# Kernel tuning notes

Measured on AMD Instinct MI355X. Metric: run time of the kernel, lower is better.

Reference implementation:

```python
import jax, jax.numpy as jnp
import numpy as np

# Regular (dv=3, dc=6) LDPC Tanner graph, rate 1/2
N = 2097152   # variable nodes (code.n)
M = 1048576   # check nodes (H.shape[0])
DV = 3
DC = 6
T = 10        # max_iterations
BC = 4        # c2v bit-width -> 2^(bc-1) = 8 magnitude levels
K = 2 ** (BC - 1)
QUANT_PARAMS = [(2.0, 1.0), (4.0, 1.5), (6.0, 2.0)]


def _make_thresholds():
    """Per-iteration threshold table [T, K]; tau_j = C*(j/(K-1))**gamma."""
    def thr(C, g):
        return [C * (j / (K - 1)) ** g for j in range(K)]
    rows = []
    for t in range(T):
        if t < T // 3:
            C, g = QUANT_PARAMS[0]
        elif t < 2 * T // 3:
            C, g = QUANT_PARAMS[1]
        else:
            C, g = QUANT_PARAMS[-1]
        rows.append(thr(C, g))
    return jnp.asarray(rows, dtype=jnp.float32)


def setup_inputs() -> dict:
    key = jax.random.key(0)
    k_llr, k_beta, k_alpha = jax.random.split(key, 3)
    rng = np.random.default_rng(0)
    # each variable node has exactly DV edges; each check exactly DC edges
    var_idx = np.repeat(np.arange(N, dtype=np.int32), DV)
    chk_idx = rng.permutation(np.repeat(np.arange(M, dtype=np.int32), DC)).astype(np.int32)
    llr = jax.random.normal(k_llr, (N,), dtype=jnp.float32) * 2.0
    # weight init matches nn.Parameter(torch.randn(1)*0.1), one per (iter, degree)
    beta = jax.random.normal(k_beta, (T,), dtype=jnp.float32) * 0.1
    alpha = jax.random.normal(k_alpha, (T,), dtype=jnp.float32) * 0.1
    return {
        "llr": llr,
        "var_idx": jnp.asarray(var_idx),
        "chk_idx": jnp.asarray(chk_idx),
        "beta": beta,
        "alpha": alpha,
        "thresholds": _make_thresholds(),
        "m": M,
    }


def reference(llr, var_idx, chk_idx, beta, alpha, thresholds, m):
    n = llr.shape[0]
    E = var_idx.shape[0]
    eidx = jnp.arange(E, dtype=jnp.int32)
    INF = jnp.float32(jnp.inf)

    def step(v2c, xs):
        b, a, thr = xs  # scalar beta_t, alpha_t, thr [K]
        neg = v2c < 0
        sgn = jnp.where(neg, -1.0, 1.0).astype(v2c.dtype)
        mag = jnp.abs(v2c)
        # --- check node update: min-sum with exclusion (min1/min2) ---
        min1 = jax.ops.segment_min(mag, chk_idx, num_segments=m)
        # first edge attaining the min in each check (ties -> lowest edge id)
        cand = jnp.where(mag <= min1[chk_idx], eidx, E)
        first = jax.ops.segment_min(cand, chk_idx, num_segments=m)
        is_min = eidx == first[chk_idx]
        min2 = jax.ops.segment_min(jnp.where(is_min, INF, mag), chk_idx, num_segments=m)
        min2 = jnp.where(jnp.isinf(min2), min1, min2)  # degree-1 guard
        # sign product excluding self: total parity * own sign
        cnt = jax.ops.segment_sum(neg.astype(jnp.int32), chk_idx, num_segments=m)
        tot = (1 - 2 * (cnt & 1)).astype(v2c.dtype)
        sign_excl = tot[chk_idx] * sgn
        mval = jnp.where(is_min, min2[chk_idx], min1[chk_idx])
        raw = b * sign_excl * mval
        # --- RCQ quantize/dequantize of c2v: snap |raw| down to threshold ---
        q = jnp.clip(jnp.searchsorted(thr, jnp.abs(raw), side="right") - 1, 0, K - 1)
        c2v = jnp.where(raw < 0, -1.0, 1.0) * thr[q]
        # --- variable node update ---
        post = llr + jax.ops.segment_sum(c2v, var_idx, num_segments=n)
        v2c_new = a * (post[var_idx] - c2v)
        return v2c_new, post

    v2c0 = llr[var_idx]
    _, posts = jax.lax.scan(step, v2c0, (beta, alpha, thresholds))
    posterior = posts[-1]
    decoded = (posterior < 0).astype(jnp.int32)
    return decoded, posterior, jnp.int32(beta.shape[0])
```

## Files before the change

kernel.cpp:

```cpp
#include <hip/hip_runtime.h>
#include <stdint.h>

#define NV 2097152
#define MC 1048576
#define EE 6291456
#define TT 10

#define CHUNK 8192
#define NBLK 768
#define FBK 512
#define CPB 2048
#define CSEG 12288
#define FG 512
#define GSEG 12288
#define VBK 256
#define VSEG 24576

__global__ __launch_bounds__(512) void initcur_kernel(uint32_t* __restrict__ gcur) {
    int i = blockIdx.x * 512 + threadIdx.x;
    gcur[i] = (uint32_t)(i & 511) * 12288u;
}

__global__ __launch_bounds__(512) void bin1_kernel(const int* __restrict__ chk_idx,
                                                   uint32_t* __restrict__ gcurA,
                                                   uint32_t* __restrict__ im1_e,
                                                   uint16_t* __restrict__ im1_c) {
    __shared__ uint32_t cnt0[512];
    __shared__ uint32_t aux[512];
    __shared__ uint32_t sA[CHUNK];
    __shared__ uint16_t sB[CHUNK];
    const int tid = threadIdx.x;
    const int rep = tid >> 8;
    const int base = blockIdx.x * CHUNK;
    cnt0[tid] = 0; aux[tid] = 0;
    __syncthreads();
    int4 cc4[4];
#pragma unroll
    for (int k = 0; k < 4; ++k) cc4[k] = ((const int4*)chk_idx)[(base >> 2) + tid + 512 * k];
    uint32_t br[16];
#pragma unroll
    for (int k = 0; k < 4; ++k) {
        int cv[4] = {cc4[k].x, cc4[k].y, cc4[k].z, cc4[k].w};
#pragma unroll
        for (int ii = 0; ii < 4; ++ii) {
            uint32_t b = (uint32_t)cv[ii] >> 11;
            uint32_t r = atomicAdd(rep ? &aux[b] : &cnt0[b], 1u);
            br[k * 4 + ii] = (b << 13) | r;
        }
    }
    __syncthreads();
    const uint32_t s0 = cnt0[tid] + aux[tid];
    aux[tid] = s0;
    __syncthreads();
    for (int d = 1; d < 512; d <<= 1) {
        uint32_t a0 = (tid >= d) ? aux[tid - d] : 0u;
        __syncthreads();
        aux[tid] += a0;
        __syncthreads();
    }
    const uint32_t excl0 = aux[tid] - s0;
    aux[tid] = excl0;
    const uint32_t gb0 = atomicAdd(&gcurA[tid], s0);
    __syncthreads();
#pragma unroll
    for (int k = 0; k < 4; ++k) {
        int cv[4] = {cc4[k].x, cc4[k].y, cc4[k].z, cc4[k].w};
#pragma unroll
        for (int ii = 0; ii < 4; ++ii) {
            uint32_t v = br[k * 4 + ii];
            uint32_t b = v >> 13;
            uint32_t r = v & 8191u;
            uint32_t j = aux[b] + (rep ? cnt0[b] : 0u) + r;
            uint32_t e = (uint32_t)(base + (tid + 512 * k) * 4 + ii);
            sA[j] = (b << 23) | e;
            sB[j] = (uint16_t)((uint32_t)cv[ii] & 2047u);
        }
    }
    __syncthreads();
    aux[tid] = gb0 - excl0;
    __syncthreads();
#pragma unroll 8
    for (int k = 0; k < 16; ++k) {
        int j = tid + 512 * k;
        uint32_t v = sA[j];
        uint32_t b = v >> 23;
        uint32_t addr = aux[b] + (uint32_t)j;
        im1_e[addr] = v & 0x7FFFFFu;
        im1_c[addr] = sB[j];
    }
}

__global__ __launch_bounds__(1024) void place1_kernel(const uint32_t* __restrict__ im1_e,
                                                      const uint16_t* __restrict__ im1_c,
                                                      uint32_t* __restrict__ chk_edges,
                                                      uint8_t* __restrict__ b1rank,
                                                      uint32_t* __restrict__ runcntB) {
    __shared__ uint32_t win[CSEG];
    __shared__ uint32_t ccnt[CPB / 2];
    __shared__ uint32_t cntB[VBK];
    const int tid = threadIdx.x, blk = blockIdx.x;
    ccnt[tid] = 0;
    if (tid < VBK) cntB[tid] = 0;
    __syncthreads();
    const size_t cb = (size_t)blk * CSEG;
    for (int k = 0; k < 3; ++k) {
        int j0 = (tid + 1024 * k) * 4;
        const uint4 e4 = *(const uint4*)&im1_e[cb + j0];
        const ushort4 c4 = *(const ushort4*)&im1_c[cb + j0];
        uint32_t c, old, s;
        c = c4.x; old = atomicAdd(&ccnt[c >> 1], 1u << ((c & 1) * 16));
        s = (old >> ((c & 1) * 16)) & 0xFFFFu; win[c * 6 + s] = e4.x;
        c = c4.y; old = atomicAdd(&ccnt[c >> 1], 1u << ((c & 1) * 16));
        s = (old >> ((c & 1) * 16)) & 0xFFFFu; win[c * 6 + s] = e4.y;
        c = c4.z; old = atomicAdd(&ccnt[c >> 1], 1u << ((c & 1) * 16));
        s = (old >> ((c & 1) * 16)) & 0xFFFFu; win[c * 6 + s] = e4.z;
        c = c4.w; old = atomicAdd(&ccnt[c >> 1], 1u << ((c & 1) * 16));
        s = (old >> ((c & 1) * 16)) & 0xFFFFu; win[c * 6 + s] = e4.w;
    }
    __syncthreads();
    for (int j = tid; j < CSEG; j += 1024) chk_edges[cb + j] = win[j];
    for (int k = 0; k < CSEG / 1024; ++k) {
        int lp = tid + 1024 * k;
        uint32_t e = win[lp];
        uint32_t bB = (e / 3u) >> 13;
        uint32_t r = atomicAdd(&cntB[bB], 1u);
        b1rank[cb + lp] = (uint8_t)r;
    }
    __syncthreads();
    if (tid < VBK) runcntB[(size_t)tid * FBK + blk] = cntB[tid];
}

__global__ __launch_bounds__(512) void bin2_kernel(const uint32_t* __restrict__ chk_edges,
                                                   uint32_t* __restrict__ gcurB,
                                                   uint32_t* __restrict__ im2_pay,
                                                   uint16_t* __restrict__ im2_el) {
    __shared__ uint32_t cnt0[512];
    __shared__ uint32_t aux[512];
    __shared__ uint32_t sA[CHUNK];
    __shared__ uint16_t sB[CHUNK];
    const int tid = threadIdx.x;
    const int rep = tid >> 8;
    const int base = blockIdx.x * CHUNK;
    cnt0[tid] = 0; aux[tid] = 0;
    __syncthreads();
    uint4 ee4[4];
#pragma unroll
    for (int k = 0; k < 4; ++k) ee4[k] = ((const uint4*)chk_edges)[(base >> 2) + tid + 512 * k];
    uint32_t br[16];
#pragma unroll
    for (int k = 0; k < 4; ++k) {
        uint32_t ev[4] = {ee4[k].x, ee4[k].y, ee4[k].z, ee4[k].w};
#pragma unroll
        for (int ii = 0; ii < 4; ++ii) {
            uint32_t vb = ev[ii] / 12288u;
            uint32_t r = atomicAdd(rep ? &aux[vb] : &cnt0[vb], 1u);
            br[k * 4 + ii] = (vb << 13) | r;
        }
    }
    __syncthreads();
    const uint32_t s0 = cnt0[tid] + aux[tid];
    aux[tid] = s0;
    __syncthreads();
    for (int d = 1; d < 512; d <<= 1) {
        uint32_t a0 = (tid >= d) ? aux[tid - d] : 0u;
        __syncthreads();
        aux[tid] += a0;
        __syncthreads();
    }
    const uint32_t excl0 = aux[tid] - s0;
    aux[tid] = excl0;
    const uint32_t gb0 = atomicAdd(&gcurB[tid], s0);
    __syncthreads();
#pragma unroll
    for (int k = 0; k < 4; ++k) {
        uint32_t ev[4] = {ee4[k].x, ee4[k].y, ee4[k].z, ee4[k].w};
#pragma unroll
        for (int ii = 0; ii < 4; ++ii) {
            uint32_t v = br[k * 4 + ii];
            uint32_t vb = v >> 13;
            uint32_t r = v & 8191u;
            uint32_t j = aux[vb] + (rep ? cnt0[vb] : 0u) + r;
            uint32_t pl = (uint32_t)((tid + 512 * k) * 4 + ii);
            sA[j] = (vb << 13) | pl;
            sB[j] = (uint16_t)(ev[ii] - vb * 12288u);
        }
    }
    __syncthreads();
    aux[tid] = gb0 - excl0;
    __syncthreads();
#pragma unroll 8
    for (int k = 0; k < 16; ++k) {
        int j = tid + 512 * k;
        uint32_t v = sA[j];
        uint32_t vb = v >> 13;
        uint32_t pos = (uint32_t)base + (v & 8191u);
        uint32_t c = pos / 6u;
        uint32_t s = pos - c * 6u;
        uint32_t addr = aux[vb] + (uint32_t)j;
        im2_pay[addr] = (c << 3) | s;
        im2_el[addr] = sB[j];
    }
}

__global__ __launch_bounds__(1024) void place2_kernel(const uint32_t* __restrict__ im2_pay,
                                                      const uint16_t* __restrict__ im2_el,
                                                      uint32_t* __restrict__ dest,
                                                      uint8_t* __restrict__ f1rank,
                                                      uint32_t* __restrict__ runcntF) {
    __shared__ uint32_t win2[GSEG];
    __shared__ uint32_t cntF[FBK];
    const int tid = threadIdx.x, g = blockIdx.x;
    if (tid < FBK) cntF[tid] = 0;
    __syncthreads();
    const size_t gb = (size_t)g * GSEG;
    for (int k = 0; k < 3; ++k) {
        int j0 = (tid + 1024 * k) * 4;
        const uint4 p4 = *(const uint4*)&im2_pay[gb + j0];
        const ushort4 e4 = *(const ushort4*)&im2_el[gb + j0];
        win2[e4.x] = p4.x; win2[e4.y] = p4.y; win2[e4.z] = p4.z; win2[e4.w] = p4.w;
    }
    __syncthreads();
    for (int j = tid; j < GSEG; j += 1024) dest[gb + j] = win2[j];
    for (int k = 0; k < GSEG / 1024; ++k) {
        int le = tid + 1024 * k;
        uint32_t b = (win2[le] >> 3) >> 11;
        uint32_t r = atomicAdd(&cntF[b], 1u);
        f1rank[gb + le] = (uint8_t)r;
    }
    __syncthreads();
    if (tid < FBK) runcntF[(size_t)tid * FG + g] = cntF[tid];
}

__global__ __launch_bounds__(256) void scanF_kernel(const uint32_t* __restrict__ runcntF,
                                                    uint32_t* __restrict__ f1base) {
    __shared__ uint32_t sc[512];
    const int tid = threadIdx.x, b = blockIdx.x;
    uint32_t c0 = runcntF[(size_t)b * FG + tid];
    uint32_t c1 = runcntF[(size_t)b * FG + tid + 256];
    sc[tid] = c0; sc[tid + 256] = c1;
    __syncthreads();
    for (int d = 1; d < 512; d <<= 1) {
        uint32_t a0 = (tid >= d) ? sc[tid - d] : 0u;
        uint32_t a1 = sc[tid + 256 - d];
        __syncthreads();
        sc[tid] += a0; sc[tid + 256] += a1;
        __syncthreads();
    }
    uint32_t base = (uint32_t)b * CSEG;
    f1base[(size_t)tid * FBK + b] = base + sc[tid] - c0;
    f1base[(size_t)(tid + 256) * FBK + b] = base + sc[tid + 256] - c1;
}

__global__ __launch_bounds__(256) void scanB_kernel(const uint32_t* __restrict__ runcntB,
                                                    uint32_t* __restrict__ b1base) {
    __shared__ uint32_t sc[512];
    const int tid = threadIdx.x, bB = blockIdx.x;
    uint32_t c0 = runcntB[(size_t)bB * FBK + tid];
    uint32_t c1 = runcntB[(size_t)bB * FBK + tid + 256];
    sc[tid] = c0; sc[tid + 256] = c1;
    __syncthreads();
    for (int d = 1; d < 512; d <<= 1) {
        uint32_t a0 = (tid >= d) ? sc[tid - d] : 0u;
        uint32_t a1 = sc[tid + 256 - d];
        __syncthreads();
        sc[tid] += a0; sc[tid + 256] += a1;
        __syncthreads();
    }
    uint32_t base = (uint32_t)bB * VSEG;
    b1base[(size_t)tid * VBK + bB] = base + sc[tid] - c0;
    b1base[(size_t)(tid + 256) * VBK + bB] = base + sc[tid + 256] - c1;
}

__global__ __launch_bounds__(1024) void fb_kernel(const uint32_t* __restrict__ dest,
                                                  const uint8_t* __restrict__ f1rank,
                                                  const uint32_t* __restrict__ runcntF,
                                                  const uint32_t* __restrict__ f1base,
                                                  uint32_t* __restrict__ goffF,
                                                  uint16_t* __restrict__ f2pos,
                                                  uint16_t* __restrict__ bidxF,
                                                  uint16_t* __restrict__ lvF) {
    __shared__ uint32_t flb[FBK];
    __shared__ uint32_t rowf[FBK];
    __shared__ uint32_t sortv[GSEG];
    const int tid = threadIdx.x, g = blockIdx.x;
    uint32_t c0 = 0;
    if (tid < FBK) {
        c0 = runcntF[(size_t)tid * FG + g];
        flb[tid] = c0;
        rowf[tid] = f1base[(size_t)g * FBK + tid];
    }
    __syncthreads();
    for (int d = 1; d < FBK; d <<= 1) {
        uint32_t a0 = 0;
        if (tid < FBK) a0 = (tid >= d) ? flb[tid - d] : 0u;
        __syncthreads();
        if (tid < FBK) flb[tid] += a0;
        __syncthreads();
    }
    if (tid < FBK) flb[tid] -= c0;
    __syncthreads();
    if (tid < FBK) goffF[(size_t)g * FBK + tid] = rowf[tid] - flb[tid];
    const size_t gb = (size_t)g * GSEG;
    for (int k = 0; k < GSEG / 1024; ++k) {
        int le = tid + 1024 * k;
        uint32_t d = dest[gb + le];
        uint32_t r = f1rank[gb + le];
        uint32_t c = d >> 3;
        uint32_t b = c >> 11;
        uint32_t pl = c * 6u + (d & 7u) - b * 12288u;
        sortv[flb[b] + r] = (b << 14) | pl;
    }
    __syncthreads();
    for (int k = 0; k < GSEG / 1024; ++k) {
        int j = tid + 1024 * k;
        uint32_t v = sortv[j];
        uint32_t b = v >> 14;
        f2pos[rowf[b] - flb[b] + j] = (uint16_t)(v & 16383u);
        bidxF[gb + j] = (uint16_t)b;
    }
    __syncthreads();
    for (int k = 0; k < GSEG / 1024; ++k) {
        int le = tid + 1024 * k;
        uint32_t d = dest[gb + le];
        uint32_t r = f1rank[gb + le];
        uint32_t b = (d >> 3) >> 11;
        uint32_t lv = (uint32_t)(le / 3);
        uint32_t sl = (uint32_t)le - 3u * lv;
        sortv[flb[b] + r] = (lv << 2) | sl;
    }
    __syncthreads();
    for (int k = 0; k < GSEG / 1024; ++k) {
        int j = tid + 1024 * k;
        lvF[gb + j] = (uint16_t)sortv[j];
    }
}

__global__ __launch_bounds__(1024) void bb_kernel(const uint32_t* __restrict__ chk_edges,
                                                  const uint8_t* __restrict__ b1rank,
                                                  const uint32_t* __restrict__ runcntB,
                                                  const uint32_t* __restrict__ b1base,
                                                  uint32_t* __restrict__ goffB,
                                                  uint16_t* __restrict__ b2pos,
                                                  uint8_t* __restrict__ bidxB,
                                                  uint16_t* __restrict__ lposB) {
    __shared__ uint32_t blb[VBK];
    __shared__ uint32_t rowb[VBK];
    __shared__ uint32_t sortv[CSEG];
    const int tid = threadIdx.x, blk = blockIdx.x;
    uint32_t c0 = 0;
    if (tid < VBK) {
        c0 = runcntB[(size_t)tid * FBK + blk];
        blb[tid] = c0;
        rowb[tid] = b1base[(size_t)blk * VBK + tid];
    }
    __syncthreads();
    for (int d = 1; d < VBK; d <<= 1) {
        uint32_t a0 = 0;
        if (tid < VBK) a0 = (tid >= d) ? blb[tid - d] : 0u;
        __syncthreads();
        if (tid < VBK) blb[tid] += a0;
        __syncthreads();
    }
    if (tid < VBK) blb[tid] -= c0;
    __syncthreads();
    if (tid < VBK) goffB[(size_t)blk * VBK + tid] = rowb[tid] - blb[tid];
    const size_t cb = (size_t)blk * CSEG;
    for (int k = 0; k < CSEG / 1024; ++k) {
        int lp = tid + 1024 * k;
        uint32_t e = chk_edges[cb + lp];
        uint32_t r = b1rank[cb + lp];
        uint32_t bB = (e / 3u) >> 13;
        uint32_t elocal = e - bB * VSEG;
        sortv[blb[bB] + r] = (bB << 15) | elocal;
    }
    __syncthreads();
    for (int k = 0; k < CSEG / 1024; ++k) {
        int j = tid + 1024 * k;
        uint32_t v = sortv[j];
        uint32_t bB = v >> 15;
        b2pos[rowb[bB] - blb[bB] + j] = (uint16_t)(v & 32767u);
        bidxB[cb + j] = (uint8_t)bB;
    }
    __syncthreads();
    for (int k = 0; k < CSEG / 1024; ++k) {
        int lp = tid + 1024 * k;
        uint32_t e = chk_edges[cb + lp];
        uint32_t r = b1rank[cb + lp];
        uint32_t bB = (e / 3u) >> 13;
        sortv[blb[bB] + r] = (uint32_t)lp;
    }
    __syncthreads();
    for (int k = 0; k < CSEG / 1024; ++k) {
        int j = tid + 1024 * k;
        lposB[cb + j] = (uint16_t)sortv[j];
    }
}

__global__ __launch_bounds__(1024) void check_kernel(const float* __restrict__ finterm,
                                                     const uint16_t* __restrict__ f2pos,
                                                     const uint16_t* __restrict__ lposB,
                                                     const uint8_t* __restrict__ bidxB,
                                                     const uint32_t* __restrict__ goffB,
                                                     uint8_t* __restrict__ binterm,
                                                     const float* __restrict__ beta,
                                                     const float* __restrict__ thresholds,
                                                     int t) {
    __shared__ __align__(16) float fwin[CSEG];
    __shared__ uint32_t grow[VBK];
    uint32_t* ewin = (uint32_t*)fwin;
    const int tid = threadIdx.x, blk = blockIdx.x;
    if (tid < VBK) grow[tid] = goffB[(size_t)blk * VBK + tid];
    const size_t cb = (size_t)blk * CSEG;
    for (int k = 0; k < 3; ++k) {
        int j0 = (tid + 1024 * k) * 4;
        const float4 f4 = *(const float4*)&finterm[cb + j0];
        const ushort4 p4 = *(const ushort4*)&f2pos[cb + j0];
        fwin[p4.x] = f4.x; fwin[p4.y] = f4.y; fwin[p4.z] = f4.z; fwin[p4.w] = f4.w;
    }
    __syncthreads();

    const float b = beta[t];
    const float* thc = thresholds + t * 8;
    const float th1 = thc[1], th2 = thc[2], th3 = thc[3], th4 = thc[4];
    const float th5 = thc[5], th6 = thc[6], th7 = thc[7];
    const uint32_t signb = (b < 0.0f) ? 1u : 0u;

    uint32_t wreg[2];
    for (int i = 0; i < 2; ++i) {
        int lc = tid + 1024 * i;
        float mags[6];
        uint32_t sgn[6];
        uint32_t parity = 0;
        uint64_t minkey = ~0ull;
#pragma unroll
        for (int j = 0; j < 6; ++j) {
            float x = fwin[lc * 6 + j];
            uint32_t s = (x < 0.0f) ? 1u : 0u;
            parity ^= s;
            sgn[j] = s;
            float mg = fabsf(x);
            mags[j] = mg;
            uint64_t key = (((uint64_t)__float_as_uint(mg)) << 3) | (uint32_t)j;
            minkey = (key < minkey) ? key : minkey;
        }
        float min1 = __uint_as_float((uint32_t)(minkey >> 3));
        uint32_t fs = (uint32_t)(minkey & 7u);
        float min2 = INFINITY;
#pragma unroll
        for (int j = 0; j < 6; ++j) {
            if ((uint32_t)j != fs) min2 = fminf(min2, mags[j]);
        }
        float m1 = fabsf(b * min1);
        float m2 = fabsf(b * min2);
        uint32_t q1 = (uint32_t)(m1 >= th1) + (uint32_t)(m1 >= th2) + (uint32_t)(m1 >= th3)
                    + (uint32_t)(m1 >= th4) + (uint32_t)(m1 >= th5) + (uint32_t)(m1 >= th6)
                    + (uint32_t)(m1 >= th7);
        uint32_t q2 = (uint32_t)(m2 >= th1) + (uint32_t)(m2 >= th2) + (uint32_t)(m2 >= th3)
                    + (uint32_t)(m2 >= th4) + (uint32_t)(m2 >= th5) + (uint32_t)(m2 >= th6)
                    + (uint32_t)(m2 >= th7);
        uint32_t w = 0;
#pragma unroll
        for (int j = 0; j < 6; ++j) {
            uint32_t neg = signb ^ parity ^ sgn[j];
            uint32_t q = ((uint32_t)j == fs) ? q2 : q1;
            w |= ((neg << 3) | q) << (4 * j);
        }
        wreg[i] = w;
    }
    __syncthreads();
    for (int i = 0; i < 2; ++i) {
        int lc = tid + 1024 * i;
        ewin[lc] = wreg[i];
    }
    __syncthreads();
    for (int k = 0; k < 3; ++k) {
        int j0 = (tid + 1024 * k) * 4;
        const ushort4 lp4 = *(const ushort4*)&lposB[cb + j0];
        const uchar4 b4 = *(const uchar4*)&bidxB[cb + j0];
        uint32_t lp, word;
        lp = lp4.x; word = ewin[lp / 6u];
        binterm[grow[b4.x] + j0 + 0] = (uint8_t)((word >> ((lp - 6u * (lp / 6u)) * 4u)) & 15u);
        lp = lp4.y; word = ewin[lp / 6u];
        binterm[grow[b4.y] + j0 + 1] = (uint8_t)((word >> ((lp - 6u * (lp / 6u)) * 4u)) & 15u);
        lp = lp4.z; word = ewin[lp / 6u];
        binterm[grow[b4.z] + j0 + 2] = (uint8_t)((word >> ((lp - 6u * (lp / 6u)) * 4u)) & 15u);
        lp = lp4.w; word = ewin[lp / 6u];
        binterm[grow[b4.w] + j0 + 3] = (uint8_t)((word >> ((lp - 6u * (lp / 6u)) * 4u)) & 15u);
    }
}

__global__ __launch_bounds__(1024) void var_kernel(const float* __restrict__ llr,
                                                   const uint8_t* __restrict__ binterm,
                                                   const uint16_t* __restrict__ b2pos,
                                                   const uint16_t* __restrict__ lvF,
                                                   const uint16_t* __restrict__ bidxF,
                                                   const uint32_t* __restrict__ goffF,
                                                   float* __restrict__ finterm,
                                                   const float* __restrict__ thresholds,
                                                   const float* __restrict__ alpha,
                                                   int t, int mode,
                                                   float* __restrict__ out) {
    __shared__ uint8_t nwin[VSEG];
    __shared__ float pwin[4096];
    __shared__ uint32_t growF[FBK];
    __shared__ float tl[8];
    const int tid = threadIdx.x, vblk = blockIdx.x;
    if (tid < 8) tl[tid] = thresholds[t * 8 + tid];
    if (mode != 1) {
        const size_t vb = (size_t)vblk * VSEG;
        for (int k = 0; k < 6; ++k) {
            int i0 = (tid + 1024 * k) * 4;
            const uchar4 n4 = *(const uchar4*)&binterm[vb + i0];
            const ushort4 p4 = *(const ushort4*)&b2pos[vb + i0];
            nwin[p4.x] = n4.x; nwin[p4.y] = n4.y; nwin[p4.z] = n4.z; nwin[p4.w] = n4.w;
        }
    }
    __syncthreads();
    const float a = (mode == 1) ? 1.0f : alpha[t];
    for (int h = 0; h < 2; ++h) {
        if (h == 1) __syncthreads();
        for (int i = 0; i < 4; ++i) {
            int lv = tid + 1024 * i;
            int lvfull = h * 4096 + lv;
            int v = vblk * 8192 + lvfull;
            float post;
            if (mode == 1) {
                post = llr[v];
            } else {
                uint32_t n0 = nwin[3 * lvfull], n1 = nwin[3 * lvfull + 1], n2 = nwin[3 * lvfull + 2];
                float c0 = (n0 & 8u) ? -tl[n0 & 7u] : tl[n0 & 7u];
                float c1 = (n1 & 8u) ? -tl[n1 & 7u] : tl[n1 & 7u];
                float c2 = (n2 & 8u) ? -tl[n2 & 7u] : tl[n2 & 7u];
                post = llr[v] + ((c0 + c1) + c2);
            }
            pwin[lv] = post;
            if (mode == 2) {
                out[v] = (post < 0.0f) ? 1.0f : 0.0f;
                out[NV + v] = post;
                if (v == 0) out[2 * NV] = 10.0f;
            }
        }
        if (mode == 2) continue;
        const int g = 2 * vblk + h;
        const int hb3 = h * 12288;
        if (tid < FBK) growF[tid] = goffF[(size_t)g * FBK + tid];
        __syncthreads();
        const size_t gb = (size_t)g * GSEG;
        for (int k = 0; k < 3; ++k) {
            int j0 = (tid + 1024 * k) * 4;
            const ushort4 lv4 = *(const ushort4*)&lvF[gb + j0];
            const ushort4 b4 = *(const ushort4*)&bidxF[gb + j0];
            float v0, v1, v2, v3;
            if (mode == 1) {
                v0 = pwin[lv4.x >> 2]; v1 = pwin[lv4.y >> 2];
                v2 = pwin[lv4.z >> 2]; v3 = pwin[lv4.w >> 2];
            } else {
                uint32_t e, lvq, nib; float c;
                e = lv4.x; lvq = e >> 2; nib = nwin[hb3 + 3 * lvq + (e & 3u)];
                c = (nib & 8u) ? -tl[nib & 7u] : tl[nib & 7u];
                v0 = a * (pwin[lvq] - c);
                e = lv4.y; lvq = e >> 2; nib = nwin[hb3 + 3 * lvq + (e & 3u)];
                c = (nib & 8u) ? -tl[nib & 7u] : tl[nib & 7u];
                v1 = a * (pwin[lvq] - c);
                e = lv4.z; lvq = e >> 2; nib = nwin[hb3 + 3 * lvq + (e & 3u)];
                c = (nib & 8u) ? -tl[nib & 7u] : tl[nib & 7u];
                v2 = a * (pwin[lvq] - c);
                e = lv4.w; lvq = e >> 2; nib = nwin[hb3 + 3 * lvq + (e & 3u)];
                c = (nib & 8u) ? -tl[nib & 7u] : tl[nib & 7u];
                v3 = a * (pwin[lvq] - c);
            }
            finterm[growF[b4.x] + j0 + 0] = v0;
            finterm[growF[b4.y] + j0 + 1] = v1;
            finterm[growF[b4.z] + j0 + 2] = v2;
            finterm[growF[b4.w] + j0 + 3] = v3;
        }
        __syncthreads();
    }
}

extern "C" void kernel_launch(void* const* d_in, const int* in_sizes, int n_in,
                              void* d_out, int out_size, void* d_ws, size_t ws_size,
                              hipStream_t stream) {
    const float* llr        = (const float*)d_in[0];
    const int*   var_idx    = (const int*)d_in[1];   (void)var_idx;
    const int*   chk_idx    = (const int*)d_in[2];
    const float* beta       = (const float*)d_in[3];
    const float* alpha      = (const float*)d_in[4];
    const float* thresholds = (const float*)d_in[5];
    float* out = (float*)d_out;

    char* wsb = (char*)d_ws;
    float*    finterm   = (float*)(wsb + 0);
    uint16_t* f2pos     = (uint16_t*)(wsb + 25165824);
    uint16_t* lvF       = (uint16_t*)(wsb + 37748736);
    uint16_t* bidxF     = (uint16_t*)(wsb + 50331648);
    uint16_t* lposB     = (uint16_t*)(wsb + 62914560);
    uint16_t* b2pos     = (uint16_t*)(wsb + 75497472);
    uint8_t*  bidxB     = (uint8_t*)(wsb + 88080384);
    uint8_t*  binterm   = (uint8_t*)(wsb + 94371840);
    uint32_t* chk_edges = (uint32_t*)(wsb + 104857600);
    uint32_t* dest      = (uint32_t*)(wsb + 130023424);
    uint32_t* im1_e     = (uint32_t*)(wsb + 155189248);
    uint16_t* im1_c     = (uint16_t*)(wsb + 180355072);
    uint32_t* im2_pay   = im1_e;
    uint16_t* im2_el    = im1_c;
    uint8_t*  f1rank    = (uint8_t*)(wsb + 192937984);
    uint8_t*  b1rank    = (uint8_t*)(wsb + 199229440);
    uint32_t* runcntF   = (uint32_t*)(wsb + 205520896);
    uint32_t* f1base    = (uint32_t*)(wsb + 206569472);
    uint32_t* runcntB   = (uint32_t*)(wsb + 207618048);
    uint32_t* b1base    = (uint32_t*)(wsb + 208142336);
    uint32_t* goffF     = (uint32_t*)(wsb + 208666624);
    uint32_t* goffB     = (uint32_t*)(wsb + 209715200);
    uint32_t* gcur      = (uint32_t*)(wsb + 210239488);
    uint32_t* gcurA     = gcur;
    uint32_t* gcurB     = gcur + 512;

    initcur_kernel<<<2, 512, 0, stream>>>(gcur);
    bin1_kernel<<<NBLK, 512, 0, stream>>>(chk_idx, gcurA, im1_e, im1_c);
    place1_kernel<<<FBK, 1024, 0, stream>>>(im1_e, im1_c, chk_edges, b1rank, runcntB);
    bin2_kernel<<<NBLK, 512, 0, stream>>>(chk_edges, gcurB, im2_pay, im2_el);
    place2_kernel<<<FG, 1024, 0, stream>>>(im2_pay, im2_el, dest, f1rank, runcntF);
    scanF_kernel<<<FBK, 256, 0, stream>>>(runcntF, f1base);
    fb_kernel<<<FG, 1024, 0, stream>>>(dest, f1rank, runcntF, f1base, goffF, f2pos, bidxF, lvF);
    scanB_kernel<<<VBK, 256, 0, stream>>>(runcntB, b1base);
    bb_kernel<<<FBK, 1024, 0, stream>>>(chk_edges, b1rank, runcntB, b1base, goffB, b2pos, bidxB, lposB);
    var_kernel<<<VBK, 1024, 0, stream>>>(llr, binterm, b2pos, lvF, bidxF, goffF,
                                         finterm, thresholds, alpha, 0, 1, out);

    for (int t = 0; t < TT; ++t) {
        check_kernel<<<FBK, 1024, 0, stream>>>(finterm, f2pos, lposB, bidxB, goffB,
                                               binterm, beta, thresholds, t);
        var_kernel<<<VBK, 1024, 0, stream>>>(llr, binterm, b2pos, lvF, bidxF, goffF,
                                             finterm, thresholds, alpha, t,
                                             (t == TT - 1) ? 2 : 0, out);
    }
}
```

Before: 618.4 us.

## Halve variable-block segment size and pack backward index/bucket into one word

```diff
diff --git a/kernel.cpp b/kernel.cpp
--- a/kernel.cpp
+++ b/kernel.cpp
@@ -13,8 +13,8 @@
 #define CSEG 12288
 #define FG 512
 #define GSEG 12288
-#define VBK 256
-#define VSEG 24576
+#define VBK 512
+#define VSEG 12288
 
 __global__ __launch_bounds__(512) void initcur_kernel(uint32_t* __restrict__ gcur) {
     int i = blockIdx.x * 512 + threadIdx.x;
@@ -122,7 +122,7 @@
     for (int k = 0; k < CSEG / 1024; ++k) {
         int lp = tid + 1024 * k;
         uint32_t e = win[lp];
-        uint32_t bB = (e / 3u) >> 13;
+        uint32_t bB = (e / 3u) >> 12;
         uint32_t r = atomicAdd(&cntB[bB], 1u);
         b1rank[cb + lp] = (uint8_t)r;
     }
@@ -341,8 +341,7 @@
                                                   const uint32_t* __restrict__ b1base,
                                                   uint32_t* __restrict__ goffB,
                                                   uint16_t* __restrict__ b2pos,
-                                                  uint8_t* __restrict__ bidxB,
-                                                  uint16_t* __restrict__ lposB) {
+                                                  uint32_t* __restrict__ bwd) {
     __shared__ uint32_t blb[VBK];
     __shared__ uint32_t rowb[VBK];
     __shared__ uint32_t sortv[CSEG];
@@ -369,37 +368,35 @@
         int lp = tid + 1024 * k;
         uint32_t e = chk_edges[cb + lp];
         uint32_t r = b1rank[cb + lp];
-        uint32_t bB = (e / 3u) >> 13;
+        uint32_t bB = (e / 3u) >> 12;
         uint32_t elocal = e - bB * VSEG;
-        sortv[blb[bB] + r] = (bB << 15) | elocal;
+        sortv[blb[bB] + r] = (bB << 14) | elocal;
     }
     __syncthreads();
     for (int k = 0; k < CSEG / 1024; ++k) {
         int j = tid + 1024 * k;
         uint32_t v = sortv[j];
-        uint32_t bB = v >> 15;
-        b2pos[rowb[bB] - blb[bB] + j] = (uint16_t)(v & 32767u);
-        bidxB[cb + j] = (uint8_t)bB;
+        uint32_t bB = v >> 14;
+        b2pos[rowb[bB] - blb[bB] + j] = (uint16_t)(v & 16383u);
     }
     __syncthreads();
     for (int k = 0; k < CSEG / 1024; ++k) {
         int lp = tid + 1024 * k;
         uint32_t e = chk_edges[cb + lp];
         uint32_t r = b1rank[cb + lp];
-        uint32_t bB = (e / 3u) >> 13;
-        sortv[blb[bB] + r] = (uint32_t)lp;
+        uint32_t bB = (e / 3u) >> 12;
+        sortv[blb[bB] + r] = (bB << 14) | (uint32_t)lp;
     }
     __syncthreads();
     for (int k = 0; k < CSEG / 1024; ++k) {
         int j = tid + 1024 * k;
-        lposB[cb + j] = (uint16_t)sortv[j];
+        bwd[cb + j] = sortv[j];
     }
 }
 
 __global__ __launch_bounds__(1024) void check_kernel(const float* __restrict__ finterm,
                                                      const uint16_t* __restrict__ f2pos,
-                                                     const uint16_t* __restrict__ lposB,
-                                                     const uint8_t* __restrict__ bidxB,
+                                                     const uint32_t* __restrict__ bwd,
                                                      const uint32_t* __restrict__ goffB,
                                                      uint8_t* __restrict__ binterm,
                                                      const float* __restrict__ beta,
@@ -475,31 +472,30 @@
     __syncthreads();
     for (int k = 0; k < 3; ++k) {
         int j0 = (tid + 1024 * k) * 4;
-        const ushort4 lp4 = *(const ushort4*)&lposB[cb + j0];
-        const uchar4 b4 = *(const uchar4*)&bidxB[cb + j0];
-        uint32_t lp, word;
-        lp = lp4.x; word = ewin[lp / 6u];
-        binterm[grow[b4.x] + j0 + 0] = (uint8_t)((word >> ((lp - 6u * (lp / 6u)) * 4u)) & 15u);
-        lp = lp4.y; word = ewin[lp / 6u];
-        binterm[grow[b4.y] + j0 + 1] = (uint8_t)((word >> ((lp - 6u * (lp / 6u)) * 4u)) & 15u);
-        lp = lp4.z; word = ewin[lp / 6u];
-        binterm[grow[b4.z] + j0 + 2] = (uint8_t)((word >> ((lp - 6u * (lp / 6u)) * 4u)) & 15u);
-        lp = lp4.w; word = ewin[lp / 6u];
-        binterm[grow[b4.w] + j0 + 3] = (uint8_t)((word >> ((lp - 6u * (lp / 6u)) * 4u)) & 15u);
-    }
-}
-
-__global__ __launch_bounds__(1024) void var_kernel(const float* __restrict__ llr,
-                                                   const uint8_t* __restrict__ binterm,
-                                                   const uint16_t* __restrict__ b2pos,
-                                                   const uint16_t* __restrict__ lvF,
-                                                   const uint16_t* __restrict__ bidxF,
-                                                   const uint32_t* __restrict__ goffF,
-                                                   float* __restrict__ finterm,
-                                                   const float* __restrict__ thresholds,
-                                                   const float* __restrict__ alpha,
-                                                   int t, int mode,
-                                                   float* __restrict__ out) {
+        const uint4 w4 = *(const uint4*)&bwd[cb + j0];
+        uint32_t w, lp, word;
+        w = w4.x; lp = w & 16383u; word = ewin[lp / 6u];
+        binterm[grow[w >> 14] + j0 + 0] = (uint8_t)((word >> ((lp - 6u * (lp / 6u)) * 4u)) & 15u);
+        w = w4.y; lp = w & 16383u; word = ewin[lp / 6u];
+        binterm[grow[w >> 14] + j0 + 1] = (uint8_t)((word >> ((lp - 6u * (lp / 6u)) * 4u)) & 15u);
+        w = w4.z; lp = w & 16383u; word = ewin[lp / 6u];
+        binterm[grow[w >> 14] + j0 + 2] = (uint8_t)((word >> ((lp - 6u * (lp / 6u)) * 4u)) & 15u);
+        w = w4.w; lp = w & 16383u; word = ewin[lp / 6u];
+        binterm[grow[w >> 14] + j0 + 3] = (uint8_t)((word >> ((lp - 6u * (lp / 6u)) * 4u)) & 15u);
+    }
+}
+
+__global__ __launch_bounds__(1024, 8) void var_kernel(const float* __restrict__ llr,
+                                                      const uint8_t* __restrict__ binterm,
+                                                      const uint16_t* __restrict__ b2pos,
+                                                      const uint16_t* __restrict__ lvF,
+                                                      const uint16_t* __restrict__ bidxF,
+                                                      const uint32_t* __restrict__ goffF,
+                                                      float* __restrict__ finterm,
+                                                      const float* __restrict__ thresholds,
+                                                      const float* __restrict__ alpha,
+                                                      int t, int mode,
+                                                      float* __restrict__ out) {
     __shared__ uint8_t nwin[VSEG];
     __shared__ float pwin[4096];
     __shared__ uint32_t growF[FBK];
@@ -508,7 +504,7 @@
     if (tid < 8) tl[tid] = thresholds[t * 8 + tid];
     if (mode != 1) {
         const size_t vb = (size_t)vblk * VSEG;
-        for (int k = 0; k < 6; ++k) {
+        for (int k = 0; k < 3; ++k) {
             int i0 = (tid + 1024 * k) * 4;
             const uchar4 n4 = *(const uchar4*)&binterm[vb + i0];
             const ushort4 p4 = *(const ushort4*)&b2pos[vb + i0];
@@ -517,64 +513,57 @@
     }
     __syncthreads();
     const float a = (mode == 1) ? 1.0f : alpha[t];
-    for (int h = 0; h < 2; ++h) {
-        if (h == 1) __syncthreads();
-        for (int i = 0; i < 4; ++i) {
-            int lv = tid + 1024 * i;
-            int lvfull = h * 4096 + lv;
-            int v = vblk * 8192 + lvfull;
-            float post;
-            if (mode == 1) {
-                post = llr[v];
-            } else {
-                uint32_t n0 = nwin[3 * lvfull], n1 = nwin[3 * lvfull + 1], n2 = nwin[3 * lvfull + 2];
-                float c0 = (n0 & 8u) ? -tl[n0 & 7u] : tl[n0 & 7u];
-                float c1 = (n1 & 8u) ? -tl[n1 & 7u] : tl[n1 & 7u];
-                float c2 = (n2 & 8u) ? -tl[n2 & 7u] : tl[n2 & 7u];
-                post = llr[v] + ((c0 + c1) + c2);
-            }
-            pwin[lv] = post;
-            if (mode == 2) {
-                out[v] = (post < 0.0f) ? 1.0f : 0.0f;
-                out[NV + v] = post;
-                if (v == 0) out[2 * NV] = 10.0f;
-            }
-        }
-        if (mode == 2) continue;
-        const int g = 2 * vblk + h;
-        const int hb3 = h * 12288;
-        if (tid < FBK) growF[tid] = goffF[(size_t)g * FBK + tid];
-        __syncthreads();
-        const size_t gb = (size_t)g * GSEG;
-        for (int k = 0; k < 3; ++k) {
-            int j0 = (tid + 1024 * k) * 4;
-            const ushort4 lv4 = *(const ushort4*)&lvF[gb + j0];
-            const ushort4 b4 = *(const ushort4*)&bidxF[gb + j0];
-            float v0, v1, v2, v3;
-            if (mode == 1) {
-                v0 = pwin[lv4.x >> 2]; v1 = pwin[lv4.y >> 2];
-                v2 = pwin[lv4.z >> 2]; v3 = pwin[lv4.w >> 2];
-            } else {
-                uint32_t e, lvq, nib; float c;
-                e = lv4.x; lvq = e >> 2; nib = nwin[hb3 + 3 * lvq + (e & 3u)];
-                c = (nib & 8u) ? -tl[nib & 7u] : tl[nib & 7u];
-                v0 = a * (pwin[lvq] - c);
-                e = lv4.y; lvq = e >> 2; nib = nwin[hb3 + 3 * lvq + (e & 3u)];
-                c = (nib & 8u) ? -tl[nib & 7u] : tl[nib & 7u];
-                v1 = a * (pwin[lvq] - c);
-                e = lv4.z; lvq = e >> 2; nib = nwin[hb3 + 3 * lvq + (e & 3u)];
-                c = (nib & 8u) ? -tl[nib & 7u] : tl[nib & 7u];
-                v2 = a * (pwin[lvq] - c);
-                e = lv4.w; lvq = e >> 2; nib = nwin[hb3 + 3 * lvq + (e & 3u)];
-                c = (nib & 8u) ? -tl[nib & 7u] : tl[nib & 7u];
-                v3 = a * (pwin[lvq] - c);
-            }
-            finterm[growF[b4.x] + j0 + 0] = v0;
-            finterm[growF[b4.y] + j0 + 1] = v1;
-            finterm[growF[b4.z] + j0 + 2] = v2;
-            finterm[growF[b4.w] + j0 + 3] = v3;
-        }
-        __syncthreads();
+    for (int i = 0; i < 4; ++i) {
+        int lv = tid + 1024 * i;
+        int v = vblk * 4096 + lv;
+        float post;
+        if (mode == 1) {
+            post = llr[v];
+        } else {
+            uint32_t n0 = nwin[3 * lv], n1 = nwin[3 * lv + 1], n2 = nwin[3 * lv + 2];
+            float c0 = (n0 & 8u) ? -tl[n0 & 7u] : tl[n0 & 7u];
+            float c1 = (n1 & 8u) ? -tl[n1 & 7u] : tl[n1 & 7u];
+            float c2 = (n2 & 8u) ? -tl[n2 & 7u] : tl[n2 & 7u];
+            post = llr[v] + ((c0 + c1) + c2);
+        }
+        pwin[lv] = post;
+        if (mode == 2) {
+            out[v] = (post < 0.0f) ? 1.0f : 0.0f;
+            out[NV + v] = post;
+            if (v == 0) out[2 * NV] = 10.0f;
+        }
+    }
+    if (mode == 2) return;
+    if (tid < FBK) growF[tid] = goffF[(size_t)vblk * FBK + tid];
+    __syncthreads();
+    const size_t gb = (size_t)vblk * GSEG;
+    for (int k = 0; k < 3; ++k) {
+        int j0 = (tid + 1024 * k) * 4;
+        const ushort4 lv4 = *(const ushort4*)&lvF[gb + j0];
+        const ushort4 b4 = *(const ushort4*)&bidxF[gb + j0];
+        float v0, v1, v2, v3;
+        if (mode == 1) {
+            v0 = pwin[lv4.x >> 2]; v1 = pwin[lv4.y >> 2];
+            v2 = pwin[lv4.z >> 2]; v3 = pwin[lv4.w >> 2];
+        } else {
+            uint32_t e, lvq, nib; float c;
+            e = lv4.x; lvq = e >> 2; nib = nwin[3 * lvq + (e & 3u)];
+            c = (nib & 8u) ? -tl[nib & 7u] : tl[nib & 7u];
+            v0 = a * (pwin[lvq] - c);
+            e = lv4.y; lvq = e >> 2; nib = nwin[3 * lvq + (e & 3u)];
+            c = (nib & 8u) ? -tl[nib & 7u] : tl[nib & 7u];
+            v1 = a * (pwin[lvq] - c);
+            e = lv4.z; lvq = e >> 2; nib = nwin[3 * lvq + (e & 3u)];
+            c = (nib & 8u) ? -tl[nib & 7u] : tl[nib & 7u];
+            v2 = a * (pwin[lvq] - c);
+            e = lv4.w; lvq = e >> 2; nib = nwin[3 * lvq + (e & 3u)];
+            c = (nib & 8u) ? -tl[nib & 7u] : tl[nib & 7u];
+            v3 = a * (pwin[lvq] - c);
+        }
+        finterm[growF[b4.x] + j0 + 0] = v0;
+        finterm[growF[b4.y] + j0 + 1] = v1;
+        finterm[growF[b4.z] + j0 + 2] = v2;
+        finterm[growF[b4.w] + j0 + 3] = v3;
     }
 }
 
@@ -594,25 +583,24 @@
     uint16_t* f2pos     = (uint16_t*)(wsb + 25165824);
     uint16_t* lvF       = (uint16_t*)(wsb + 37748736);
     uint16_t* bidxF     = (uint16_t*)(wsb + 50331648);
-    uint16_t* lposB     = (uint16_t*)(wsb + 62914560);
-    uint16_t* b2pos     = (uint16_t*)(wsb + 75497472);
-    uint8_t*  bidxB     = (uint8_t*)(wsb + 88080384);
-    uint8_t*  binterm   = (uint8_t*)(wsb + 94371840);
-    uint32_t* chk_edges = (uint32_t*)(wsb + 104857600);
-    uint32_t* dest      = (uint32_t*)(wsb + 130023424);
-    uint32_t* im1_e     = (uint32_t*)(wsb + 155189248);
-    uint16_t* im1_c     = (uint16_t*)(wsb + 180355072);
+    uint32_t* bwd       = (uint32_t*)(wsb + 62914560);
+    uint16_t* b2pos     = (uint16_t*)(wsb + 88080384);
+    uint8_t*  binterm   = (uint8_t*)(wsb + 100663296);
+    uint32_t* chk_edges = (uint32_t*)(wsb + 106954752);
+    uint32_t* dest      = (uint32_t*)(wsb + 132120576);
+    uint32_t* im1_e     = (uint32_t*)(wsb + 157286400);
+    uint16_t* im1_c     = (uint16_t*)(wsb + 182452224);
     uint32_t* im2_pay   = im1_e;
     uint16_t* im2_el    = im1_c;
-    uint8_t*  f1rank    = (uint8_t*)(wsb + 192937984);
-    uint8_t*  b1rank    = (uint8_t*)(wsb + 199229440);
-    uint32_t* runcntF   = (uint32_t*)(wsb + 205520896);
-    uint32_t* f1base    = (uint32_t*)(wsb + 206569472);
-    uint32_t* runcntB   = (uint32_t*)(wsb + 207618048);
-    uint32_t* b1base    = (uint32_t*)(wsb + 208142336);
-    uint32_t* goffF     = (uint32_t*)(wsb + 208666624);
-    uint32_t* goffB     = (uint32_t*)(wsb + 209715200);
-    uint32_t* gcur      = (uint32_t*)(wsb + 210239488);
+    uint8_t*  f1rank    = (uint8_t*)(wsb + 195035136);
+    uint8_t*  b1rank    = (uint8_t*)(wsb + 201326592);
+    uint32_t* runcntF   = (uint32_t*)(wsb + 207618048);
+    uint32_t* f1base    = (uint32_t*)(wsb + 208666624);
+    uint32_t* runcntB   = (uint32_t*)(wsb + 209715200);
+    uint32_t* b1base    = (uint32_t*)(wsb + 210763776);
+    uint32_t* goffF     = (uint32_t*)(wsb + 211812352);
+    uint32_t* goffB     = (uint32_t*)(wsb + 212860928);
+    uint32_t* gcur      = (uint32_t*)(wsb + 213909504);
     uint32_t* gcurA     = gcur;
     uint32_t* gcurB     = gcur + 512;
 
@@ -624,12 +612,12 @@
     scanF_kernel<<<FBK, 256, 0, stream>>>(runcntF, f1base);
     fb_kernel<<<FG, 1024, 0, stream>>>(dest, f1rank, runcntF, f1base, goffF, f2pos, bidxF, lvF);
     scanB_kernel<<<VBK, 256, 0, stream>>>(runcntB, b1base);
-    bb_kernel<<<FBK, 1024, 0, stream>>>(chk_edges, b1rank, runcntB, b1base, goffB, b2pos, bidxB, lposB);
+    bb_kernel<<<FBK, 1024, 0, stream>>>(chk_edges, b1rank, runcntB, b1base, goffB, b2pos, bwd);
     var_kernel<<<VBK, 1024, 0, stream>>>(llr, binterm, b2pos, lvF, bidxF, goffF,
                                          finterm, thresholds, alpha, 0, 1, out);
 
     for (int t = 0; t < TT; ++t) {
-        check_kernel<<<FBK, 1024, 0, stream>>>(finterm, f2pos, lposB, bidxB, goffB,
+        check_kernel<<<FBK, 1024, 0, stream>>>(finterm, f2pos, bwd, goffB,
                                                binterm, beta, thresholds, t);
         var_kernel<<<VBK, 1024, 0, stream>>>(llr, binterm, b2pos, lvF, bidxF, goffF,
                                              finterm, thresholds, alpha, t,
```

After: 642.4 us. 3.9% more time.

## Double variable-block count to 512 with half-size segments per block

Applied to the files above, without the earlier changes.

```diff
diff --git a/kernel.cpp b/kernel.cpp
--- a/kernel.cpp
+++ b/kernel.cpp
@@ -13,8 +13,8 @@
 #define CSEG 12288
 #define FG 512
 #define GSEG 12288
-#define VBK 256
-#define VSEG 24576
+#define VBK 512
+#define VSEG 12288
 
 __global__ __launch_bounds__(512) void initcur_kernel(uint32_t* __restrict__ gcur) {
     int i = blockIdx.x * 512 + threadIdx.x;
@@ -122,7 +122,7 @@
     for (int k = 0; k < CSEG / 1024; ++k) {
         int lp = tid + 1024 * k;
         uint32_t e = win[lp];
-        uint32_t bB = (e / 3u) >> 13;
+        uint32_t bB = (e / 3u) >> 12;
         uint32_t r = atomicAdd(&cntB[bB], 1u);
         b1rank[cb + lp] = (uint8_t)r;
     }
@@ -340,6 +340,7 @@
                                                   const uint32_t* __restrict__ runcntB,
                                                   const uint32_t* __restrict__ b1base,
                                                   uint32_t* __restrict__ goffB,
+                                                  uint32_t* __restrict__ jsplit,
                                                   uint16_t* __restrict__ b2pos,
                                                   uint8_t* __restrict__ bidxB,
                                                   uint16_t* __restrict__ lposB) {
@@ -364,29 +365,29 @@
     if (tid < VBK) blb[tid] -= c0;
     __syncthreads();
     if (tid < VBK) goffB[(size_t)blk * VBK + tid] = rowb[tid] - blb[tid];
+    if (tid == 0) jsplit[blk] = blb[256];
     const size_t cb = (size_t)blk * CSEG;
     for (int k = 0; k < CSEG / 1024; ++k) {
         int lp = tid + 1024 * k;
         uint32_t e = chk_edges[cb + lp];
         uint32_t r = b1rank[cb + lp];
-        uint32_t bB = (e / 3u) >> 13;
+        uint32_t bB = (e / 3u) >> 12;
         uint32_t elocal = e - bB * VSEG;
-        sortv[blb[bB] + r] = (bB << 15) | elocal;
+        sortv[blb[bB] + r] = (bB << 14) | elocal;
     }
     __syncthreads();
     for (int k = 0; k < CSEG / 1024; ++k) {
         int j = tid + 1024 * k;
         uint32_t v = sortv[j];
-        uint32_t bB = v >> 15;
-        b2pos[rowb[bB] - blb[bB] + j] = (uint16_t)(v & 32767u);
-        bidxB[cb + j] = (uint8_t)bB;
+        b2pos[(size_t)rowb[v >> 14] - blb[v >> 14] + j] = (uint16_t)(v & 16383u);
+        bidxB[cb + j] = (uint8_t)(v >> 14);
     }
     __syncthreads();
     for (int k = 0; k < CSEG / 1024; ++k) {
         int lp = tid + 1024 * k;
         uint32_t e = chk_edges[cb + lp];
         uint32_t r = b1rank[cb + lp];
-        uint32_t bB = (e / 3u) >> 13;
+        uint32_t bB = (e / 3u) >> 12;
         sortv[blb[bB] + r] = (uint32_t)lp;
     }
     __syncthreads();
@@ -401,6 +402,7 @@
                                                      const uint16_t* __restrict__ lposB,
                                                      const uint8_t* __restrict__ bidxB,
                                                      const uint32_t* __restrict__ goffB,
+                                                     const uint32_t* __restrict__ jsplit,
                                                      uint8_t* __restrict__ binterm,
                                                      const float* __restrict__ beta,
                                                      const float* __restrict__ thresholds,
@@ -410,6 +412,7 @@
     uint32_t* ewin = (uint32_t*)fwin;
     const int tid = threadIdx.x, blk = blockIdx.x;
     if (tid < VBK) grow[tid] = goffB[(size_t)blk * VBK + tid];
+    const uint32_t js = jsplit[blk];
     const size_t cb = (size_t)blk * CSEG;
     for (int k = 0; k < 3; ++k) {
         int j0 = (tid + 1024 * k) * 4;
@@ -477,15 +480,19 @@
         int j0 = (tid + 1024 * k) * 4;
         const ushort4 lp4 = *(const ushort4*)&lposB[cb + j0];
         const uchar4 b4 = *(const uchar4*)&bidxB[cb + j0];
-        uint32_t lp, word;
+        uint32_t lp, word, bB;
         lp = lp4.x; word = ewin[lp / 6u];
-        binterm[grow[b4.x] + j0 + 0] = (uint8_t)((word >> ((lp - 6u * (lp / 6u)) * 4u)) & 15u);
+        bB = (uint32_t)b4.x + (((uint32_t)(j0 + 0) >= js) ? 256u : 0u);
+        binterm[grow[bB] + j0 + 0] = (uint8_t)((word >> ((lp - 6u * (lp / 6u)) * 4u)) & 15u);
         lp = lp4.y; word = ewin[lp / 6u];
-        binterm[grow[b4.y] + j0 + 1] = (uint8_t)((word >> ((lp - 6u * (lp / 6u)) * 4u)) & 15u);
+        bB = (uint32_t)b4.y + (((uint32_t)(j0 + 1) >= js) ? 256u : 0u);
+        binterm[grow[bB] + j0 + 1] = (uint8_t)((word >> ((lp - 6u * (lp / 6u)) * 4u)) & 15u);
         lp = lp4.z; word = ewin[lp / 6u];
-        binterm[grow[b4.z] + j0 + 2] = (uint8_t)((word >> ((lp - 6u * (lp / 6u)) * 4u)) & 15u);
+        bB = (uint32_t)b4.z + (((uint32_t)(j0 + 2) >= js) ? 256u : 0u);
+        binterm[grow[bB] + j0 + 2] = (uint8_t)((word >> ((lp - 6u * (lp / 6u)) * 4u)) & 15u);
         lp = lp4.w; word = ewin[lp / 6u];
-        binterm[grow[b4.w] + j0 + 3] = (uint8_t)((word >> ((lp - 6u * (lp / 6u)) * 4u)) & 15u);
+        bB = (uint32_t)b4.w + (((uint32_t)(j0 + 3) >= js) ? 256u : 0u);
+        binterm[grow[bB] + j0 + 3] = (uint8_t)((word >> ((lp - 6u * (lp / 6u)) * 4u)) & 15u);
     }
 }
 
@@ -508,7 +515,7 @@
     if (tid < 8) tl[tid] = thresholds[t * 8 + tid];
     if (mode != 1) {
         const size_t vb = (size_t)vblk * VSEG;
-        for (int k = 0; k < 6; ++k) {
+        for (int k = 0; k < 3; ++k) {
             int i0 = (tid + 1024 * k) * 4;
             const uchar4 n4 = *(const uchar4*)&binterm[vb + i0];
             const ushort4 p4 = *(const ushort4*)&b2pos[vb + i0];
@@ -517,64 +524,57 @@
     }
     __syncthreads();
     const float a = (mode == 1) ? 1.0f : alpha[t];
-    for (int h = 0; h < 2; ++h) {
-        if (h == 1) __syncthreads();
-        for (int i = 0; i < 4; ++i) {
-            int lv = tid + 1024 * i;
-            int lvfull = h * 4096 + lv;
-            int v = vblk * 8192 + lvfull;
-            float post;
-            if (mode == 1) {
-                post = llr[v];
-            } else {
-                uint32_t n0 = nwin[3 * lvfull], n1 = nwin[3 * lvfull + 1], n2 = nwin[3 * lvfull + 2];
-                float c0 = (n0 & 8u) ? -tl[n0 & 7u] : tl[n0 & 7u];
-                float c1 = (n1 & 8u) ? -tl[n1 & 7u] : tl[n1 & 7u];
-                float c2 = (n2 & 8u) ? -tl[n2 & 7u] : tl[n2 & 7u];
-                post = llr[v] + ((c0 + c1) + c2);
-            }
-            pwin[lv] = post;
-            if (mode == 2) {
-                out[v] = (post < 0.0f) ? 1.0f : 0.0f;
-                out[NV + v] = post;
-                if (v == 0) out[2 * NV] = 10.0f;
-            }
-        }
-        if (mode == 2) continue;
-        const int g = 2 * vblk + h;
-        const int hb3 = h * 12288;
-        if (tid < FBK) growF[tid] = goffF[(size_t)g * FBK + tid];
-        __syncthreads();
-        const size_t gb = (size_t)g * GSEG;
-        for (int k = 0; k < 3; ++k) {
-            int j0 = (tid + 1024 * k) * 4;
-            const ushort4 lv4 = *(const ushort4*)&lvF[gb + j0];
-            const ushort4 b4 = *(const ushort4*)&bidxF[gb + j0];
-            float v0, v1, v2, v3;
-            if (mode == 1) {
-                v0 = pwin[lv4.x >> 2]; v1 = pwin[lv4.y >> 2];
-                v2 = pwin[lv4.z >> 2]; v3 = pwin[lv4.w >> 2];
-            } else {
-                uint32_t e, lvq, nib; float c;
-                e = lv4.x; lvq = e >> 2; nib = nwin[hb3 + 3 * lvq + (e & 3u)];
-                c = (nib & 8u) ? -tl[nib & 7u] : tl[nib & 7u];
-                v0 = a * (pwin[lvq] - c);
-                e = lv4.y; lvq = e >> 2; nib = nwin[hb3 + 3 * lvq + (e & 3u)];
-                c = (nib & 8u) ? -tl[nib & 7u] : tl[nib & 7u];
-                v1 = a * (pwin[lvq] - c);
-                e = lv4.z; lvq = e >> 2; nib = nwin[hb3 + 3 * lvq + (e & 3u)];
-                c = (nib & 8u) ? -tl[nib & 7u] : tl[nib & 7u];
-                v2 = a * (pwin[lvq] - c);
-                e = lv4.w; lvq = e >> 2; nib = nwin[hb3 + 3 * lvq + (e & 3u)];
-                c = (nib & 8u) ? -tl[nib & 7u] : tl[nib & 7u];
-                v3 = a * (pwin[lvq] - c);
-            }
-            finterm[growF[b4.x] + j0 + 0] = v0;
-            finterm[growF[b4.y] + j0 + 1] = v1;
-            finterm[growF[b4.z] + j0 + 2] = v2;
-            finterm[growF[b4.w] + j0 + 3] = v3;
-        }
-        __syncthreads();
+    for (int i = 0; i < 4; ++i) {
+        int lv = tid + 1024 * i;
+        int v = vblk * 4096 + lv;
+        float post;
+        if (mode == 1) {
+            post = llr[v];
+        } else {
+            uint32_t n0 = nwin[3 * lv], n1 = nwin[3 * lv + 1], n2 = nwin[3 * lv + 2];
+            float c0 = (n0 & 8u) ? -tl[n0 & 7u] : tl[n0 & 7u];
+            float c1 = (n1 & 8u) ? -tl[n1 & 7u] : tl[n1 & 7u];
+            float c2 = (n2 & 8u) ? -tl[n2 & 7u] : tl[n2 & 7u];
+            post = llr[v] + ((c0 + c1) + c2);
+        }
+        pwin[lv] = post;
+        if (mode == 2) {
+            out[v] = (post < 0.0f) ? 1.0f : 0.0f;
+            out[NV + v] = post;
+            if (v == 0) out[2 * NV] = 10.0f;
+        }
+    }
+    if (mode == 2) return;
+    if (tid < FBK) growF[tid] = goffF[(size_t)vblk * FBK + tid];
+    __syncthreads();
+    const size_t gb = (size_t)vblk * GSEG;
+    for (int k = 0; k < 3; ++k) {
+        int j0 = (tid + 1024 * k) * 4;
+        const ushort4 lv4 = *(const ushort4*)&lvF[gb + j0];
+        const ushort4 b4 = *(const ushort4*)&bidxF[gb + j0];
+        float v0, v1, v2, v3;
+        if (mode == 1) {
+            v0 = pwin[lv4.x >> 2]; v1 = pwin[lv4.y >> 2];
+            v2 = pwin[lv4.z >> 2]; v3 = pwin[lv4.w >> 2];
+        } else {
+            uint32_t e, lvq, nib; float c;
+            e = lv4.x; lvq = e >> 2; nib = nwin[3 * lvq + (e & 3u)];
+            c = (nib & 8u) ? -tl[nib & 7u] : tl[nib & 7u];
+            v0 = a * (pwin[lvq] - c);
+            e = lv4.y; lvq = e >> 2; nib = nwin[3 * lvq + (e & 3u)];
+            c = (nib & 8u) ? -tl[nib & 7u] : tl[nib & 7u];
+            v1 = a * (pwin[lvq] - c);
+            e = lv4.z; lvq = e >> 2; nib = nwin[3 * lvq + (e & 3u)];
+            c = (nib & 8u) ? -tl[nib & 7u] : tl[nib & 7u];
+            v2 = a * (pwin[lvq] - c);
+            e = lv4.w; lvq = e >> 2; nib = nwin[3 * lvq + (e & 3u)];
+            c = (nib & 8u) ? -tl[nib & 7u] : tl[nib & 7u];
+            v3 = a * (pwin[lvq] - c);
+        }
+        finterm[growF[b4.x] + j0 + 0] = v0;
+        finterm[growF[b4.y] + j0 + 1] = v1;
+        finterm[growF[b4.z] + j0 + 2] = v2;
+        finterm[growF[b4.w] + j0 + 3] = v3;
     }
 }
 
@@ -609,10 +609,11 @@
     uint32_t* runcntF   = (uint32_t*)(wsb + 205520896);
     uint32_t* f1base    = (uint32_t*)(wsb + 206569472);
     uint32_t* runcntB   = (uint32_t*)(wsb + 207618048);
-    uint32_t* b1base    = (uint32_t*)(wsb + 208142336);
-    uint32_t* goffF     = (uint32_t*)(wsb + 208666624);
-    uint32_t* goffB     = (uint32_t*)(wsb + 209715200);
-    uint32_t* gcur      = (uint32_t*)(wsb + 210239488);
+    uint32_t* b1base    = (uint32_t*)(wsb + 208666624);
+    uint32_t* goffF     = (uint32_t*)(wsb + 209715200);
+    uint32_t* goffB     = (uint32_t*)(wsb + 210763776);
+    uint32_t* jsplit    = (uint32_t*)(wsb + 211812352);
+    uint32_t* gcur      = (uint32_t*)(wsb + 211814400);
     uint32_t* gcurA     = gcur;
     uint32_t* gcurB     = gcur + 512;
 
@@ -624,12 +625,13 @@
     scanF_kernel<<<FBK, 256, 0, stream>>>(runcntF, f1base);
     fb_kernel<<<FG, 1024, 0, stream>>>(dest, f1rank, runcntF, f1base, goffF, f2pos, bidxF, lvF);
     scanB_kernel<<<VBK, 256, 0, stream>>>(runcntB, b1base);
-    bb_kernel<<<FBK, 1024, 0, stream>>>(chk_edges, b1rank, runcntB, b1base, goffB, b2pos, bidxB, lposB);
+    bb_kernel<<<FBK, 1024, 0, stream>>>(chk_edges, b1rank, runcntB, b1base, goffB, jsplit,
+                                        b2pos, bidxB, lposB);
     var_kernel<<<VBK, 1024, 0, stream>>>(llr, binterm, b2pos, lvF, bidxF, goffF,
                                          finterm, thresholds, alpha, 0, 1, out);
 
     for (int t = 0; t < TT; ++t) {
-        check_kernel<<<FBK, 1024, 0, stream>>>(finterm, f2pos, lposB, bidxB, goffB,
+        check_kernel<<<FBK, 1024, 0, stream>>>(finterm, f2pos, lposB, bidxB, goffB, jsplit,
                                                binterm, beta, thresholds, t);
         var_kernel<<<VBK, 1024, 0, stream>>>(llr, binterm, b2pos, lvF, bidxF, goffF,
                                              finterm, thresholds, alpha, t,
```

After: 638.2 us. +3.2%, slower.
